# Optimization experiments

Hardware: AMD Instinct MI355X
Metric: run time of the kernel (lower is better)

## Reference

```python
import jax, jax.numpy as jnp
import numpy as np

HIDDEN = 4096
NQ = 32        # query heads
NKV = 8        # kv heads
HD = 128       # head dim
EPS = 1e-6
BASE = 10000.0
T = 2048


def setup_inputs() -> dict:
    key = jax.random.key(0)
    ks = jax.random.split(key, 4)
    s = 0.02
    return {
        "hidden_states": jax.random.normal(ks[0], (T, HIDDEN), jnp.float32),
        "w_qkv": jax.random.normal(ks[1], ((NQ + 2 * NKV) * HD, HIDDEN), jnp.float32) * s,
        "q_norm_w": jnp.ones((HD,), jnp.float32),
        "k_norm_w": jnp.ones((HD,), jnp.float32),
        "w_o": jax.random.normal(ks[2], (HIDDEN, NQ * HD), jnp.float32) * s,
        "positions": jnp.arange(T, dtype=jnp.int64),
    }


def _rms_norm(x, w):
    # x: [T, H, D], normalize over last dim
    var = jnp.mean(jnp.square(x), axis=-1, keepdims=True)
    return x * jax.lax.rsqrt(var + EPS) * w


def _rope(x, positions):
    # neox-style: split halves. x: [T, H, D]
    half = HD // 2
    inv_freq = 1.0 / (BASE ** (jnp.arange(0, HD, 2, dtype=jnp.float32) / HD))  # [half]
    ang = positions.astype(jnp.float32)[:, None] * inv_freq  # [T, half]
    cos = jnp.cos(ang)[:, None, :]  # [T, 1, half]
    sin = jnp.sin(ang)[:, None, :]
    x1, x2 = x[..., :half], x[..., half:]
    return jnp.concatenate([x1 * cos - x2 * sin, x2 * cos + x1 * sin], axis=-1)


def reference(hidden_states, w_qkv, q_norm_w, k_norm_w, w_o, positions):
    t = hidden_states.shape[0]
    qkv = hidden_states @ w_qkv.T  # [T, (NQ+2*NKV)*HD]
    q, k, v = jnp.split(qkv, [NQ * HD, (NQ + NKV) * HD], axis=-1)
    q = _rms_norm(q.reshape(t, NQ, HD), q_norm_w)
    k = _rms_norm(k.reshape(t, NKV, HD), k_norm_w)
    v = v.reshape(t, NKV, HD)
    q = _rope(q, positions)
    k = _rope(k, positions)

    g = NQ // NKV
    qg = q.reshape(t, NKV, g, HD).transpose(1, 2, 0, 3)  # [NKV, g, T, HD]
    kt = k.transpose(1, 0, 2)  # [NKV, T, HD]
    vt = v.transpose(1, 0, 2)
    scale = HD ** -0.5
    scores = jnp.einsum('hgqd,hkd->hgqk', qg, kt) * scale  # [NKV, g, T, T]
    causal = positions[:, None] >= positions[None, :]  # [T, T]
    scores = jnp.where(causal[None, None], scores, jnp.float32(-1e30))
    p = jax.nn.softmax(scores, axis=-1)
    o = jnp.einsum('hgqk,hkd->hgqd', p, vt)  # [NKV, g, T, HD]
    o = o.transpose(2, 0, 1, 3).reshape(t, NQ * HD)
    return o @ w_o.T
```

## Files before the change

kernel.cpp:

```cpp
#include <hip/hip_runtime.h>
#include <hip/hip_bf16.h>

typedef float f32x4 __attribute__((ext_vector_type(4)));
typedef short s16x8 __attribute__((ext_vector_type(8)));
typedef short s16x4 __attribute__((ext_vector_type(4)));
typedef unsigned short u16;

#define HIDDEN 4096
#define NQ 32
#define NKV 8
#define HD 128
#define T_SEQ 2048
#define QKV_N ((NQ + 2 * NKV) * HD)

__device__ __forceinline__ u16 f2bf(float f) {
    union { float f; unsigned u; } v; v.f = f;
    unsigned r = v.u + 0x7FFFu + ((v.u >> 16) & 1u);
    return (u16)(r >> 16);
}
__device__ __forceinline__ float b2f(u16 h) {
    union { unsigned u; float f; } v; v.u = ((unsigned)h) << 16; return v.f;
}
__device__ __forceinline__ void gload_lds16(const u16* g, u16* l) {
    __builtin_amdgcn_global_load_lds(
        (const __attribute__((address_space(1))) unsigned int*)g,
        (__attribute__((address_space(3))) unsigned int*)l,
        16, 0, 0);
}
__device__ __forceinline__ int xcd_swz(int flat, int nwg) {
    return (flat & 7) * (nwg >> 3) + (flat >> 3);
}

__global__ __launch_bounds__(256) void conv_bf16_kern(
    const float* __restrict__ src, u16* __restrict__ dst, int n8)
{
    for (int i = blockIdx.x * 256 + threadIdx.x; i < n8; i += gridDim.x * 256) {
        const float4 a = ((const float4*)src)[2 * i];
        const float4 b = ((const float4*)src)[2 * i + 1];
        s16x8 o;
        o[0] = (short)f2bf(a.x); o[1] = (short)f2bf(a.y);
        o[2] = (short)f2bf(a.z); o[3] = (short)f2bf(a.w);
        o[4] = (short)f2bf(b.x); o[5] = (short)f2bf(b.y);
        o[6] = (short)f2bf(b.z); o[7] = (short)f2bf(b.w);
        ((s16x8*)dst)[i] = o;
    }
}

template<int OUT_BF16>
__global__ __launch_bounds__(256) void gemm_bt_bf16(
    const u16* __restrict__ A, const u16* __restrict__ B,
    void* __restrict__ Cv, int N, int K)
{
    __shared__ u16 As[2][128 * 32];
    __shared__ u16 Bs[2][128 * 32];
    const int tid = threadIdx.x, lane = tid & 63, wid = tid >> 6;
    const int wr = wid >> 1, wc = wid & 1, lg = lane >> 4, l15 = lane & 15;
    const int nwg = gridDim.x * gridDim.y;
    const int flat = xcd_swz((int)blockIdx.y * gridDim.x + (int)blockIdx.x, nwg);
    const int m0 = (flat / gridDim.x) * 128, n0 = (flat % gridDim.x) * 128;
    const int srow = wid * 32 + (lane >> 2);
    const int scol = (((lane & 3) ^ ((lane >> 3) & 3))) * 8;
    const u16* ga = &A[(size_t)(m0 + srow) * K + scol];
    const u16* gb = &B[(size_t)(n0 + srow) * K + scol];
    const int rsw = (lg ^ ((l15 >> 1) & 3)) * 8;

    f32x4 acc[4][4] = {};
    const int nk = K >> 5;

    auto stage = [&](int buf, int koff) {
        u16* la = &As[buf][wid * 1024];
        u16* lb = &Bs[buf][wid * 1024];
        gload_lds16(ga + koff, la);
        gload_lds16(ga + koff + 16 * K, la + 512);
        gload_lds16(gb + koff, lb);
        gload_lds16(gb + koff + 16 * K, lb + 512);
    };

    stage(0, 0);
    for (int kk = 0; kk < nk; ++kk) {
        const int cur = kk & 1;
        if (kk + 1 < nk) {
            stage(cur ^ 1, (kk + 1) * 32);
            asm volatile("s_waitcnt vmcnt(4)" ::: "memory");
        } else {
            asm volatile("s_waitcnt vmcnt(0)" ::: "memory");
        }
        __builtin_amdgcn_s_barrier();
        s16x8 af[4], bfr[4];
#pragma unroll
        for (int i = 0; i < 4; ++i) af[i]  = *(const s16x8*)&As[cur][(wr * 64 + i * 16 + l15) * 32 + rsw];
#pragma unroll
        for (int j = 0; j < 4; ++j) bfr[j] = *(const s16x8*)&Bs[cur][(wc * 64 + j * 16 + l15) * 32 + rsw];
#pragma unroll
        for (int i = 0; i < 4; ++i)
#pragma unroll
            for (int j = 0; j < 4; ++j)
                acc[i][j] = __builtin_amdgcn_mfma_f32_16x16x32_bf16(af[i], bfr[j], acc[i][j], 0, 0, 0);
        __builtin_amdgcn_s_barrier();
    }
#pragma unroll
    for (int i = 0; i < 4; ++i) {
        int r0 = m0 + wr * 64 + i * 16 + lg * 4;
#pragma unroll
        for (int j = 0; j < 4; ++j) {
            int cc = n0 + wc * 64 + j * 16 + l15;
#pragma unroll
            for (int r = 0; r < 4; ++r) {
                if (OUT_BF16)
                    ((u16*)Cv)[(size_t)(r0 + r) * N + cc] = f2bf(acc[i][j][r]);
                else
                    ((float*)Cv)[(size_t)(r0 + r) * N + cc] = acc[i][j][r];
            }
        }
    }
}

__global__ __launch_bounds__(256) void norm_rope_kern(
    const u16* __restrict__ qkv, const float* __restrict__ qw,
    const float* __restrict__ kw, u16* __restrict__ qr, u16* __restrict__ kr)
{
    const int t = blockIdx.x, h = blockIdx.y * 4 + (threadIdx.x >> 6);
    const int i = threadIdx.x & 63;
    const size_t rowbase = (size_t)t * QKV_N;
    const u16* src; const float* w; u16* dst;
    if (h < 32) {
        src = qkv + rowbase + h * HD; w = qw;
        dst = qr + ((size_t)h * T_SEQ + t) * HD;
    } else {
        int kh = h - 32;
        src = qkv + rowbase + NQ * HD + kh * HD; w = kw;
        dst = kr + ((size_t)kh * T_SEQ + t) * HD;
    }
    float x1 = b2f(src[i]), x2 = b2f(src[i + 64]);
    float ss = x1 * x1 + x2 * x2;
#pragma unroll
    for (int d = 32; d >= 1; d >>= 1) ss += __shfl_xor(ss, d);
    float rs = rsqrtf(ss * (1.0f / 128.0f) + 1e-6f);
    x1 *= rs * w[i];
    x2 *= rs * w[i + 64];
    float ang = (float)t * powf(10000.0f, -(float)i * (1.0f / 64.0f));
    float sn, cs;
    sincosf(ang, &sn, &cs);
    dst[i]      = f2bf(x1 * cs - x2 * sn);
    dst[i + 64] = f2bf(x2 * cs + x1 * sn);
}

__global__ __launch_bounds__(256) void vtrans_kern(
    const u16* __restrict__ qkv, u16* __restrict__ vt)
{
    __shared__ u16 Ts[128][66];
    const int t0 = blockIdx.x * 64, kh = blockIdx.y, tid = threadIdx.x;
#pragma unroll
    for (int it = 0; it < 4; ++it) {
        int slot = tid + it * 256;
        int tl = slot >> 4, dc = (slot & 15) * 8;
        s16x8 v = *(const s16x8*)&qkv[(size_t)(t0 + tl) * QKV_N + (NQ + NKV) * HD + kh * HD + dc];
#pragma unroll
        for (int e = 0; e < 8; ++e) Ts[dc + e][tl] = (u16)v[e];
    }
    __syncthreads();
#pragma unroll
    for (int it = 0; it < 4; ++it) {
        int slot = tid + it * 256;
        int d = slot >> 3, c = (slot & 7) * 8;
        s16x8 v = *(const s16x8*)&Ts[d][c];
        *(s16x8*)&vt[((size_t)kh * HD + d) * T_SEQ + t0 + c] = v;
    }
}

#define KS(r, c) Ks[((r) << 7) + ((c) ^ (((r) & 7) << 3))]
#define VS(r, c) Vs[((r) << 6) + ((c) ^ (((r) & 7) << 3))]
#define PS(wv, r, c) Ps[((wv) << 10) + ((r) << 6) + ((c) ^ (((r) & 7) << 3))]

__global__ __launch_bounds__(512) void attn_kern(
    const u16* __restrict__ qr, const u16* __restrict__ kr,
    const u16* __restrict__ vt, u16* __restrict__ o)
{
    __shared__ u16 Ks[64 * 128];
    __shared__ u16 Vs[128 * 64];
    __shared__ u16 Ps[8 * 16 * 64];
    const int tid = threadIdx.x, lane = tid & 63, w = tid >> 6;
    const int lg = lane >> 4, l15 = lane & 15;
    const int flat = xcd_swz((int)blockIdx.y * 8 + (int)blockIdx.x, 256);
    const int qh = flat >> 3, bx = flat & 7;
    const int kvh = qh >> 2;
    const float scale2 = 0.08838834764831845f * 1.4426950408889634f;

    const int krow = tid >> 4, kcol = (tid & 15) * 8;
    const int vrow = tid >> 3, vcol = (tid & 7) * 8;
    const u16* krbase = kr + (size_t)kvh * T_SEQ * HD;
    const u16* vtbase = vt + (size_t)kvh * HD * T_SEQ;

    s16x8 kst[2], vst[2];
#define LOADKV(k0_) do { \
    kst[0] = *(const s16x8*)&krbase[(size_t)((k0_) + krow) * HD + kcol]; \
    kst[1] = *(const s16x8*)&krbase[(size_t)((k0_) + krow + 32) * HD + kcol]; \
    vst[0] = *(const s16x8*)&vtbase[(size_t)(vrow) * T_SEQ + (k0_) + vcol]; \
    vst[1] = *(const s16x8*)&vtbase[(size_t)(vrow + 64) * T_SEQ + (k0_) + vcol]; \
    } while (0)

    for (int half = 0; half < 2; ++half) {
        const int q0 = (half == 0) ? bx * 128 : (T_SEQ - 128) - bx * 128;
        s16x8 qf[4];
        {
            const u16* qb = qr + ((size_t)qh * T_SEQ + q0 + w * 16 + l15) * HD;
#pragma unroll
            for (int dc = 0; dc < 4; ++dc) qf[dc] = *(const s16x8*)&qb[dc * 32 + lg * 8];
        }
        f32x4 oacc[8] = {};
        float mQ = -1e30f, lsQ = 0.f;

        const int ktiles = (q0 >> 6) + 2;
        LOADKV(0);
        for (int kt = 0; kt < ktiles; ++kt) {
            const int k0 = kt * 64;
            __syncthreads();
            *(s16x8*)&KS(krow, kcol) = kst[0];
            *(s16x8*)&KS(krow + 32, kcol) = kst[1];
            *(s16x8*)&VS(vrow, vcol) = vst[0];
            *(s16x8*)&VS(vrow + 64, vcol) = vst[1];
            __syncthreads();
            if (kt + 1 < ktiles) LOADKV(k0 + 64);

            f32x4 sc[4] = {};
            __builtin_amdgcn_s_setprio(1);
#pragma unroll
            for (int nc = 0; nc < 4; ++nc)
#pragma unroll
                for (int dc = 0; dc < 4; ++dc) {
                    s16x8 kf = *(const s16x8*)&KS(nc * 16 + l15, dc * 32 + lg * 8);
                    sc[nc] = __builtin_amdgcn_mfma_f32_16x16x32_bf16(kf, qf[dc], sc[nc], 0, 0, 0);
                }
            __builtin_amdgcn_s_setprio(0);

            const int qg = q0 + w * 16 + l15;
            const bool needMask = (k0 + 63) > (q0 + w * 16);
            float tm = -1e30f;
#pragma unroll
            for (int nc = 0; nc < 4; ++nc)
#pragma unroll
                for (int r = 0; r < 4; ++r) {
                    float v = sc[nc][r] * scale2;
                    int kg = k0 + nc * 16 + lg * 4 + r;
                    if (needMask && kg > qg) v = -1e30f;
                    sc[nc][r] = v;
                    tm = fmaxf(tm, v);
                }
            tm = fmaxf(tm, __shfl_xor(tm, 16));
            tm = fmaxf(tm, __shfl_xor(tm, 32));

            if (__any(tm > mQ + 8.0f)) {
                float mn = fmaxf(mQ, tm);
                float alpha = exp2f(mQ - mn);
                mQ = mn;
                lsQ *= alpha;
                float aq[4];
#pragma unroll
                for (int r = 0; r < 4; ++r) aq[r] = __shfl(alpha, lg * 4 + r);
#pragma unroll
                for (int dc = 0; dc < 8; ++dc)
#pragma unroll
                    for (int r = 0; r < 4; ++r) oacc[dc][r] *= aq[r];
            }

            float ts = 0.f;
#pragma unroll
            for (int nc = 0; nc < 4; ++nc) {
                s16x4 pk;
#pragma unroll
                for (int r = 0; r < 4; ++r) {
                    float e = exp2f(sc[nc][r] - mQ);
                    ts += e;
                    pk[r] = (short)f2bf(e);
                }
                *(s16x4*)&PS(w, l15, nc * 16 + lg * 4) = pk;
            }
            ts += __shfl_xor(ts, 16);
            ts += __shfl_xor(ts, 32);
            lsQ += ts;

            __builtin_amdgcn_s_setprio(1);
#pragma unroll
            for (int kc = 0; kc < 2; ++kc) {
                s16x8 pf = *(const s16x8*)&PS(w, l15, kc * 32 + lg * 8);
#pragma unroll
                for (int dc = 0; dc < 8; ++dc) {
                    s16x8 vf = *(const s16x8*)&VS(dc * 16 + l15, kc * 32 + lg * 8);
                    oacc[dc] = __builtin_amdgcn_mfma_f32_16x16x32_bf16(pf, vf, oacc[dc], 0, 0, 0);
                }
            }
            __builtin_amdgcn_s_setprio(0);
        }
        float lq[4];
#pragma unroll
        for (int r = 0; r < 4; ++r) lq[r] = __shfl(lsQ, lg * 4 + r);
#pragma unroll
        for (int r = 0; r < 4; ++r) {
            float inv = 1.0f / lq[r];
            int trow = q0 + w * 16 + lg * 4 + r;
            u16* dst = o + (size_t)trow * (NQ * HD) + qh * HD;
#pragma unroll
            for (int dc = 0; dc < 8; ++dc) dst[dc * 16 + l15] = f2bf(oacc[dc][r] * inv);
        }
    }
#undef LOADKV
}

extern "C" void kernel_launch(void* const* d_in, const int* in_sizes, int n_in,
                              void* d_out, int out_size, void* d_ws, size_t ws_size,
                              hipStream_t stream)
{
    const float* hs   = (const float*)d_in[0];
    const float* wqkv = (const float*)d_in[1];
    const float* qw   = (const float*)d_in[2];
    const float* kw   = (const float*)d_in[3];
    const float* wo   = (const float*)d_in[4];
    float* out = (float*)d_out;

    char* ws = (char*)d_ws;
    u16* hs_bf   = (u16*)(ws);
    u16* ob      = (u16*)(ws);
    u16* wqkv_bf = (u16*)(ws + 16777216);
    u16* qr      = (u16*)(ws + 16777216);
    u16* kr      = (u16*)(ws + 33554432);
    u16* vt      = (u16*)(ws + 37748736);
    u16* wo_bf   = (u16*)(ws + 41943040);
    u16* qkv_bf  = (u16*)(ws + 67108864);

    conv_bf16_kern<<<2048, 256, 0, stream>>>(hs, hs_bf, T_SEQ * HIDDEN / 8);
    conv_bf16_kern<<<2048, 256, 0, stream>>>(wqkv, wqkv_bf, QKV_N * HIDDEN / 8);
    gemm_bt_bf16<1><<<dim3(QKV_N / 128, T_SEQ / 128), 256, 0, stream>>>(
        hs_bf, wqkv_bf, (void*)qkv_bf, QKV_N, HIDDEN);
    norm_rope_kern<<<dim3(T_SEQ, 10), 256, 0, stream>>>(qkv_bf, qw, kw, qr, kr);
    vtrans_kern<<<dim3(T_SEQ / 64, NKV), 256, 0, stream>>>(qkv_bf, vt);
    conv_bf16_kern<<<2048, 256, 0, stream>>>(wo, wo_bf, HIDDEN * HIDDEN / 8);
    attn_kern<<<dim3(8, NQ), 512, 0, stream>>>(qr, kr, vt, ob);
    gemm_bt_bf16<0><<<dim3(HIDDEN / 128, T_SEQ / 128), 256, 0, stream>>>(
        ob, wo_bf, (void*)out, HIDDEN, HIDDEN);
}
```

Baseline: 366.2 us.

## Double-buffer attention K/V tiles, merge bf16 conversions, drop GEMM XCD swizzle

The attention kernel now double-buffers its K/V shared-memory tiles, so the next tile is written to the spare buffer after the PV MFMAs and each iteration needs one barrier instead of two. The two fp32-to-bf16 conversion launches are merged into a single kernel. The GEMM tile mapping drops the XCD swizzle in favour of a plain blockIdx mapping, which may change L2 locality across XCDs. RoPE frequencies are computed with exp2f instead of powf. Shared memory per attention block doubles for K/V, which may reduce occupancy.

```diff
diff --git a/kernel.cpp b/kernel.cpp
--- a/kernel.cpp
+++ b/kernel.cpp
@@ -31,18 +31,29 @@
     return (flat & 7) * (nwg >> 3) + (flat >> 3);
 }
 
+__device__ __forceinline__ void conv8(const float* src, u16* dst, int i) {
+    const float4 a = ((const float4*)src)[2 * i];
+    const float4 b = ((const float4*)src)[2 * i + 1];
+    s16x8 o;
+    o[0] = (short)f2bf(a.x); o[1] = (short)f2bf(a.y);
+    o[2] = (short)f2bf(a.z); o[3] = (short)f2bf(a.w);
+    o[4] = (short)f2bf(b.x); o[5] = (short)f2bf(b.y);
+    o[6] = (short)f2bf(b.z); o[7] = (short)f2bf(b.w);
+    ((s16x8*)dst)[i] = o;
+}
 __global__ __launch_bounds__(256) void conv_bf16_kern(
     const float* __restrict__ src, u16* __restrict__ dst, int n8)
 {
-    for (int i = blockIdx.x * 256 + threadIdx.x; i < n8; i += gridDim.x * 256) {
-        const float4 a = ((const float4*)src)[2 * i];
-        const float4 b = ((const float4*)src)[2 * i + 1];
-        s16x8 o;
-        o[0] = (short)f2bf(a.x); o[1] = (short)f2bf(a.y);
-        o[2] = (short)f2bf(a.z); o[3] = (short)f2bf(a.w);
-        o[4] = (short)f2bf(b.x); o[5] = (short)f2bf(b.y);
-        o[6] = (short)f2bf(b.z); o[7] = (short)f2bf(b.w);
-        ((s16x8*)dst)[i] = o;
+    for (int i = blockIdx.x * 256 + threadIdx.x; i < n8; i += gridDim.x * 256)
+        conv8(src, dst, i);
+}
+__global__ __launch_bounds__(256) void conv2_bf16_kern(
+    const float* __restrict__ s1, u16* __restrict__ d1, int n1,
+    const float* __restrict__ s2, u16* __restrict__ d2, int n2)
+{
+    for (int i = blockIdx.x * 256 + threadIdx.x; i < n1 + n2; i += gridDim.x * 256) {
+        if (i < n1) conv8(s1, d1, i);
+        else        conv8(s2, d2, i - n1);
     }
 }
 
@@ -55,9 +66,7 @@
     __shared__ u16 Bs[2][128 * 32];
     const int tid = threadIdx.x, lane = tid & 63, wid = tid >> 6;
     const int wr = wid >> 1, wc = wid & 1, lg = lane >> 4, l15 = lane & 15;
-    const int nwg = gridDim.x * gridDim.y;
-    const int flat = xcd_swz((int)blockIdx.y * gridDim.x + (int)blockIdx.x, nwg);
-    const int m0 = (flat / gridDim.x) * 128, n0 = (flat % gridDim.x) * 128;
+    const int m0 = blockIdx.y * 128, n0 = blockIdx.x * 128;
     const int srow = wid * 32 + (lane >> 2);
     const int scol = (((lane & 3) ^ ((lane >> 3) & 3))) * 8;
     const u16* ga = &A[(size_t)(m0 + srow) * K + scol];
@@ -138,7 +147,7 @@
     float rs = rsqrtf(ss * (1.0f / 128.0f) + 1e-6f);
     x1 *= rs * w[i];
     x2 *= rs * w[i + 64];
-    float ang = (float)t * powf(10000.0f, -(float)i * (1.0f / 64.0f));
+    float ang = (float)t * exp2f((float)i * -0.20762050593567985f);
     float sn, cs;
     sincosf(ang, &sn, &cs);
     dst[i]      = f2bf(x1 * cs - x2 * sn);
@@ -168,16 +177,16 @@
     }
 }
 
-#define KS(r, c) Ks[((r) << 7) + ((c) ^ (((r) & 7) << 3))]
-#define VS(r, c) Vs[((r) << 6) + ((c) ^ (((r) & 7) << 3))]
+#define KS(b, r, c) Ks[(b)][((r) << 7) + ((c) ^ (((r) & 7) << 3))]
+#define VS(b, r, c) Vs[(b)][((r) << 6) + ((c) ^ (((r) & 7) << 3))]
 #define PS(wv, r, c) Ps[((wv) << 10) + ((r) << 6) + ((c) ^ (((r) & 7) << 3))]
 
 __global__ __launch_bounds__(512) void attn_kern(
     const u16* __restrict__ qr, const u16* __restrict__ kr,
     const u16* __restrict__ vt, u16* __restrict__ o)
 {
-    __shared__ u16 Ks[64 * 128];
-    __shared__ u16 Vs[128 * 64];
+    __shared__ u16 Ks[2][64 * 128];
+    __shared__ u16 Vs[2][128 * 64];
     __shared__ u16 Ps[8 * 16 * 64];
     const int tid = threadIdx.x, lane = tid & 63, w = tid >> 6;
     const int lg = lane >> 4, l15 = lane & 15;
@@ -198,6 +207,12 @@
     vst[0] = *(const s16x8*)&vtbase[(size_t)(vrow) * T_SEQ + (k0_) + vcol]; \
     vst[1] = *(const s16x8*)&vtbase[(size_t)(vrow + 64) * T_SEQ + (k0_) + vcol]; \
     } while (0)
+#define WRITEKV(b) do { \
+    *(s16x8*)&KS((b), krow, kcol) = kst[0]; \
+    *(s16x8*)&KS((b), krow + 32, kcol) = kst[1]; \
+    *(s16x8*)&VS((b), vrow, vcol) = vst[0]; \
+    *(s16x8*)&VS((b), vrow + 64, vcol) = vst[1]; \
+    } while (0)
 
     for (int half = 0; half < 2; ++half) {
         const int q0 = (half == 0) ? bx * 128 : (T_SEQ - 128) - bx * 128;
@@ -212,14 +227,11 @@
 
         const int ktiles = (q0 >> 6) + 2;
         LOADKV(0);
+        WRITEKV(0);
+        __syncthreads();
         for (int kt = 0; kt < ktiles; ++kt) {
             const int k0 = kt * 64;
-            __syncthreads();
-            *(s16x8*)&KS(krow, kcol) = kst[0];
-            *(s16x8*)&KS(krow + 32, kcol) = kst[1];
-            *(s16x8*)&VS(vrow, vcol) = vst[0];
-            *(s16x8*)&VS(vrow + 64, vcol) = vst[1];
-            __syncthreads();
+            const int cur = kt & 1;
             if (kt + 1 < ktiles) LOADKV(k0 + 64);
 
             f32x4 sc[4] = {};
@@ -228,7 +240,7 @@
             for (int nc = 0; nc < 4; ++nc)
 #pragma unroll
                 for (int dc = 0; dc < 4; ++dc) {
-                    s16x8 kf = *(const s16x8*)&KS(nc * 16 + l15, dc * 32 + lg * 8);
+                    s16x8 kf = *(const s16x8*)&KS(cur, nc * 16 + l15, dc * 32 + lg * 8);
                     sc[nc] = __builtin_amdgcn_mfma_f32_16x16x32_bf16(kf, qf[dc], sc[nc], 0, 0, 0);
                 }
             __builtin_amdgcn_s_setprio(0);
@@ -285,11 +297,14 @@
                 s16x8 pf = *(const s16x8*)&PS(w, l15, kc * 32 + lg * 8);
 #pragma unroll
                 for (int dc = 0; dc < 8; ++dc) {
-                    s16x8 vf = *(const s16x8*)&VS(dc * 16 + l15, kc * 32 + lg * 8);
+                    s16x8 vf = *(const s16x8*)&VS(cur, dc * 16 + l15, kc * 32 + lg * 8);
                     oacc[dc] = __builtin_amdgcn_mfma_f32_16x16x32_bf16(pf, vf, oacc[dc], 0, 0, 0);
                 }
             }
             __builtin_amdgcn_s_setprio(0);
+
+            if (kt + 1 < ktiles) WRITEKV(cur ^ 1);
+            __syncthreads();
         }
         float lq[4];
 #pragma unroll
@@ -304,6 +319,7 @@
         }
     }
 #undef LOADKV
+#undef WRITEKV
 }
 
 extern "C" void kernel_launch(void* const* d_in, const int* in_sizes, int n_in,
@@ -327,8 +343,8 @@
     u16* wo_bf   = (u16*)(ws + 41943040);
     u16* qkv_bf  = (u16*)(ws + 67108864);
 
-    conv_bf16_kern<<<2048, 256, 0, stream>>>(hs, hs_bf, T_SEQ * HIDDEN / 8);
-    conv_bf16_kern<<<2048, 256, 0, stream>>>(wqkv, wqkv_bf, QKV_N * HIDDEN / 8);
+    conv2_bf16_kern<<<2048, 256, 0, stream>>>(
+        hs, hs_bf, T_SEQ * HIDDEN / 8, wqkv, wqkv_bf, QKV_N * HIDDEN / 8);
     gemm_bt_bf16<1><<<dim3(QKV_N / 128, T_SEQ / 128), 256, 0, stream>>>(
         hs_bf, wqkv_bf, (void*)qkv_bf, QKV_N, HIDDEN);
     norm_rope_kern<<<dim3(T_SEQ, 10), 256, 0, stream>>>(qkv_bf, qw, kw, qr, kr);
```

Measured after the change: 349.9 us. -4.4%, faster.
